# Kernel tuning notes

Measured on AMD Instinct MI355X. Metric: run time of the kernel, lower is better.

## Reference

```python
import jax, jax.numpy as jnp
import numpy as np

B, T, DM, H, HD = 2, 2048, 1024, 16, 64

def _rope_cos_sin(t, hd):
    inv_freq = 1.0 / (10000.0 ** (jnp.arange(0, hd, 2, dtype=jnp.float32) / hd))
    ang = jnp.arange(t, dtype=jnp.float32)[:, None] * inv_freq[None, :]  # [T, hd/2]
    emb = jnp.concatenate([ang, ang], axis=-1)  # [T, hd]
    return jnp.cos(emb), jnp.sin(emb)

def setup_inputs() -> dict:
    key = jax.random.key(0)
    kx, kq, kp = jax.random.split(key, 3)
    x = jax.random.normal(kx, (B, T, DM), dtype=jnp.float32)
    cos, sin = _rope_cos_sin(T, HD)
    w_qkv = jax.random.normal(kq, (3 * DM, DM), dtype=jnp.float32) * (DM ** -0.5)
    w_proj = jax.random.normal(kp, (DM, DM), dtype=jnp.float32) * (DM ** -0.5)
    return {"x": x, "cos": cos, "sin": sin, "w_qkv": w_qkv, "w_proj": w_proj}

def _rotate_half(u):
    d = u.shape[-1] // 2
    return jnp.concatenate([-u[..., d:], u[..., :d]], axis=-1)

def _apply_rope(u, cos, sin):
    # u: [B, T, H, D]; cos/sin: [T, D] -> unsqueeze_dim=1 -> [T, 1, D]
    c = cos[:, None, :]
    s = sin[:, None, :]
    return u * c + _rotate_half(u) * s

def reference(x, cos, sin, w_qkv, w_proj):
    b, t, _ = x.shape
    qkv = jnp.einsum('btd,ed->bte', x, w_qkv)            # [B, T, 3*DM]
    qkv = qkv.reshape(b, t, 3, H, HD)
    q, k, v = qkv[:, :, 0], qkv[:, :, 1], qkv[:, :, 2]   # each [B, T, H, HD]
    q = _apply_rope(q, cos, sin)
    k = _apply_rope(k, cos, sin)
    q = q.transpose(0, 2, 1, 3)                          # [B, H, T, HD]
    k = k.transpose(0, 2, 1, 3)
    v = v.transpose(0, 2, 1, 3)
    scale = 1.0 / jnp.sqrt(jnp.float32(HD))
    scores = jnp.einsum('bhqd,bhkd->bhqk', q, k) * scale  # [B, H, T, T]
    causal = jnp.tril(jnp.ones((t, t), dtype=bool))
    scores = jnp.where(causal[None, None], scores, jnp.finfo(scores.dtype).min)
    attn = jax.nn.softmax(scores, axis=-1)
    out = jnp.einsum('bhqk,bhkd->bhqd', attn, v)          # [B, H, T, HD]
    out = out.transpose(0, 2, 1, 3).reshape(b, t, H * HD)
    return jnp.einsum('btd,ed->bte', out, w_proj)
```

## Files before the change

### kernel.cpp

```cpp
#include <hip/hip_runtime.h>
#include <stdint.h>

#define Bb 2
#define Tt 2048
#define DMm 1024
#define Hh 16
#define HDd 64
#define Mrows (Bb*Tt)

typedef __attribute__((ext_vector_type(8)))  __bf16 bf16x8;
typedef __attribute__((ext_vector_type(4)))  __bf16 bf16x4;
typedef __attribute__((ext_vector_type(4)))  float  f32x4;
typedef __attribute__((ext_vector_type(16))) float  f32x16;
typedef __attribute__((ext_vector_type(4)))  unsigned int u32x4;
typedef __attribute__((ext_vector_type(2)))  unsigned int u32x2;

#define GLD16(gp, lp) __builtin_amdgcn_global_load_lds( \
    (const __attribute__((address_space(1))) unsigned int*)(gp), \
    (__attribute__((address_space(3))) unsigned int*)(lp), 16, 0, 0)

static __device__ __forceinline__ unsigned cvtpk_bf16(float lo, float hi) {
  unsigned r;
  asm("v_cvt_pk_bf16_f32 %0, %1, %2" : "=v"(r) : "v"(lo), "v"(hi));
  return r;
}
static __device__ __forceinline__ float exp2_hw(float x) {
  float r;
  asm("v_exp_f32 %0, %1" : "=v"(r) : "v"(x));
  return r;
}
static __device__ __forceinline__ float fmax3(float a, float b, float c) {
  return fmaxf(fmaxf(a, b), c);
}
static __device__ __forceinline__ float xmax32(float v) {
  return fmaxf(v, __shfl_xor(v, 32));
}
static __device__ __forceinline__ float xsum32(float v) {
  return v + __shfl_xor(v, 32);
}

__global__ __launch_bounds__(256)
void cast3_k(const float* __restrict__ a, const float* __restrict__ b,
             const float* __restrict__ c,
             __bf16* __restrict__ oa, __bf16* __restrict__ ob,
             __bf16* __restrict__ oc,
             const float* __restrict__ cosb, const float* __restrict__ sinb,
             unsigned* __restrict__ cs) {
  const int NA = 1048576, NB = 786432, NC = 262144;
  int i = blockIdx.x * 256 + threadIdx.x;
  if (i < NA + NB + NC) {
    const float* src; __bf16* dst; int k;
    if (i < NA)            { src = a; dst = oa; k = i; }
    else if (i < NA + NB)  { src = b; dst = ob; k = i - NA; }
    else                   { src = c; dst = oc; k = i - NA - NB; }
    float4 v = ((const float4*)src)[k];
    bf16x4 o;
    o[0] = (__bf16)v.x; o[1] = (__bf16)v.y; o[2] = (__bf16)v.z; o[3] = (__bf16)v.w;
    ((bf16x4*)dst)[k] = o;
  } else {
    int k = i - (NA + NB + NC);
    cs[k] = cvtpk_bf16(cosb[k], sinb[k]);
  }
}

__global__ __launch_bounds__(256)
void gemm_bt(const __bf16* __restrict__ A, const __bf16* __restrict__ Bm,
             float* __restrict__ C) {
  const int N = 1024, K = 1024;
  __shared__ __bf16 As[128 * 32];
  __shared__ __bf16 Bs[64 * 32];
  const int bid = blockIdx.x;
  const int xcd = bid & 7, i2 = bid >> 3;
  const int rowBase = (xcd * 4 + (i2 & 3)) * 128;
  const int colBase = (i2 >> 2) * 64;
  const int tid  = threadIdx.x;
  const int lane = tid & 63, wid = tid >> 6;
  const int l4 = lane & 15, lhi = lane >> 4;
  const int wh = wid >> 1, ww = wid & 1;
  f32x4 acc[4][2] = {};
  const int e0 = wid * 512 + lane * 8;
  const int r0 = e0 >> 5, c0 = e0 & 31;
  const __bf16* a0 = A  + (size_t)(rowBase + r0)      * K + c0;
  const __bf16* a1 = A  + (size_t)(rowBase + r0 + 64) * K + c0;
  const __bf16* b0 = Bm + (size_t)(colBase + r0)      * K + c0;
  for (int k0 = 0; k0 < K; k0 += 32) {
    __syncthreads();
    GLD16(a0 + k0, &As[wid * 512]);
    GLD16(a1 + k0, &As[2048 + wid * 512]);
    GLD16(b0 + k0, &Bs[wid * 512]);
    __syncthreads();
    bf16x8 af[4], bfr[2];
#pragma unroll
    for (int i = 0; i < 4; i++)
      af[i]  = *(const bf16x8*)&As[(wh * 64 + i * 16 + l4) * 32 + lhi * 8];
#pragma unroll
    for (int j = 0; j < 2; j++)
      bfr[j] = *(const bf16x8*)&Bs[(ww * 32 + j * 16 + l4) * 32 + lhi * 8];
#pragma unroll
    for (int i = 0; i < 4; i++)
#pragma unroll
      for (int j = 0; j < 2; j++)
        acc[i][j] = __builtin_amdgcn_mfma_f32_16x16x32_bf16(af[i], bfr[j], acc[i][j], 0, 0, 0);
  }
#pragma unroll
  for (int i = 0; i < 4; i++) {
    int R = rowBase + wh * 64 + i * 16 + lhi * 4;
#pragma unroll
    for (int j = 0; j < 2; j++) {
      int Cc = colBase + ww * 32 + j * 16 + l4;
      float* cp = C + (size_t)R * N + Cc;
#pragma unroll
      for (int q = 0; q < 4; q++) cp[(size_t)q * N] = acc[i][j][q];
    }
  }
}

__global__ __launch_bounds__(256)
void gemm_qkv(const __bf16* __restrict__ A, const __bf16* __restrict__ Bm,
              __bf16* __restrict__ Qb, __bf16* __restrict__ Kb,
              __bf16* __restrict__ Vfb, const unsigned* __restrict__ csb) {
  const int K = 1024;
  __shared__ __bf16 ldsu[16384];
  __bf16* As = ldsu;
  __bf16* Bs = ldsu + 4096;
  const int bid = blockIdx.x;
  const int xcd = bid & 7, i2 = bid >> 3;
  const int rowBase = (xcd * 4 + (i2 & 3)) * 128;
  const int colBase = (i2 >> 2) * 128;
  const int tid  = threadIdx.x;
  const int lane = tid & 63, wid = tid >> 6;
  const int l4 = lane & 15, lhi = lane >> 4;
  const int wh = wid >> 1, ww = wid & 1;
  f32x4 acc[4][4] = {};
  const int e0 = wid * 512 + lane * 8;
  const int r0 = e0 >> 5, c0 = e0 & 31;
  const __bf16* a0 = A  + (size_t)(rowBase + r0)      * K + c0;
  const __bf16* a1 = A  + (size_t)(rowBase + r0 + 64) * K + c0;
  const __bf16* b0 = Bm + (size_t)(colBase + r0)      * K + c0;
  const __bf16* b1 = Bm + (size_t)(colBase + r0 + 64) * K + c0;
  for (int k0 = 0; k0 < K; k0 += 32) {
    __syncthreads();
    GLD16(a0 + k0, &As[wid * 512]);
    GLD16(a1 + k0, &As[2048 + wid * 512]);
    GLD16(b0 + k0, &Bs[wid * 512]);
    GLD16(b1 + k0, &Bs[2048 + wid * 512]);
    __syncthreads();
    bf16x8 af[4], bfr[4];
#pragma unroll
    for (int i = 0; i < 4; i++) {
      af[i]  = *(const bf16x8*)&As[(wh * 64 + i * 16 + l4) * 32 + lhi * 8];
      bfr[i] = *(const bf16x8*)&Bs[(ww * 64 + i * 16 + l4) * 32 + lhi * 8];
    }
#pragma unroll
    for (int i = 0; i < 4; i++)
#pragma unroll
      for (int j = 0; j < 4; j++)
        acc[i][j] = __builtin_amdgcn_mfma_f32_16x16x32_bf16(af[i], bfr[j], acc[i][j], 0, 0, 0);
  }

  const int region = colBase >> 10;
  const int base_h = (colBase & 1023) >> 6;
  const int bIdx   = rowBase >> 11;
  const int tileBase = (rowBase & 2047) >> 5;

  __syncthreads();

  if (region < 2) {
    const float qscale = region ? 1.f : 0.18033688f;
#pragma unroll
    for (int i = 0; i < 4; i++) {
      const int tbase = ww * 8192 + (wh * 2 + (i >> 1)) * 2048;
      const int rsub  = (i & 1) * 16 + lhi * 4;
      const int trow0 = (rowBase & 2047) + wh * 64 + i * 16 + lhi * 4;
#pragma unroll
      for (int j = 0; j < 4; j++) {
        int dd = j * 16 + l4;
        float sg = (j < 2) ? -1.f : 1.f;
        int lbase = tbase + j * 512 + (l4 >> 3) * 256 + (l4 & 7);
#pragma unroll
        for (int q = 0; q < 4; q++) {
          unsigned cw = csb[(trow0 + q) * 64 + dd];
          float cc = __builtin_bit_cast(float, cw << 16);
          float sn = __builtin_bit_cast(float, cw & 0xffff0000u);
          float r = (acc[i][j][q] * cc + sg * acc[i][j ^ 2][q] * sn) * qscale;
          ldsu[lbase + (rsub + q) * 8] = (__bf16)r;
        }
      }
    }
  } else {
#pragma unroll
    for (int i = 0; i < 4; i++) {
      const int tbase = ww * 8192 + (wh * 2 + (i >> 1)) * 2048 + (i & 1) * 512;
#pragma unroll
      for (int j = 0; j < 4; j++) {
        int lbase = tbase + (j >> 1) * 1024 + ((j & 1) * 16 + l4) * 8;
#pragma unroll
        for (int q = 0; q < 4; q++) {
          int rq = lhi * 4 + q;
          ldsu[lbase + ((rq >> 3) & 1) * 256 + (rq & 7)] = (__bf16)acc[i][j][q];
        }
      }
    }
  }
  __syncthreads();

  __bf16* dstBuf = (region == 0) ? Qb : (region == 1 ? Kb : Vfb);
#pragma unroll
  for (int h2 = 0; h2 < 2; ++h2) {
    __bf16* dst = dstBuf + (size_t)(bIdx * 16 + base_h + h2) * (Tt * 64)
                + (size_t)tileBase * 2048;
#pragma unroll
    for (int k = 0; k < 4; ++k) {
      int eoff = k * 2048 + tid * 8;
      *(bf16x8*)(dst + eoff) = *(const bf16x8*)&ldsu[h2 * 8192 + eoff];
    }
  }
}

__global__ __launch_bounds__(256)
void attn_k(const __bf16* __restrict__ Q, const __bf16* __restrict__ K,
            const __bf16* __restrict__ Vb, __bf16* __restrict__ O) {
  const int bid = blockIdx.x;
  const int xcd = bid & 7;
  const int ii  = bid >> 3;
  const int bh  = xcd * 4 + (ii & 3);
  const int jj  = ii >> 2;
  const int b = bh >> 4, h = bh & 15;
  const int tid = threadIdx.x, lane = tid & 63, w = tid >> 6;
  const int l5 = lane & 31, hi = lane >> 5;
  const size_t baseF = (size_t)bh * (Tt * 64);
  const int laneoff = (hi << 8) + (l5 << 3);
  const float NEG_INF = -__builtin_inff();

  __shared__ float  oL[4][32][65];
  __shared__ float2 msL[4][32];

#define FRAGP(P, tile, c) ((P) + baseF + (size_t)(((tile) * 4 + (c)) << 9) + laneoff)

#define LOADK(KA, TIX) do {                                               \
    KA[0] = *(const bf16x8*)FRAGP(K, (TIX), 0);                           \
    KA[1] = *(const bf16x8*)FRAGP(K, (TIX), 1);                           \
    KA[2] = *(const bf16x8*)FRAGP(K, (TIX), 2);                           \
    KA[3] = *(const bf16x8*)FRAGP(K, (TIX), 3);                           \
  } while (0)
#define LOADV(TIX) do {                                                   \
    vc[0] = *(const bf16x8*)FRAGP(Vb, (TIX), 0);                          \
    vc[1] = *(const bf16x8*)FRAGP(Vb, (TIX), 1);                          \
    vc[2] = *(const bf16x8*)FRAGP(Vb, (TIX), 2);                          \
    vc[3] = *(const bf16x8*)FRAGP(Vb, (TIX), 3);                          \
  } while (0)

#define COMPUTE(KA, TIX) do {                                             \
    f32x16 s = {};                                                        \
    __builtin_amdgcn_s_setprio(1);                                        \
    s = __builtin_amdgcn_mfma_f32_32x32x16_bf16(KA[0], qf[0], s, 0, 0, 0);\
    s = __builtin_amdgcn_mfma_f32_32x32x16_bf16(KA[1], qf[1], s, 0, 0, 0);\
    s = __builtin_amdgcn_mfma_f32_32x32x16_bf16(KA[2], qf[2], s, 0, 0, 0);\
    s = __builtin_amdgcn_mfma_f32_32x32x16_bf16(KA[3], qf[3], s, 0, 0, 0);\
    __builtin_amdgcn_s_setprio(0);                                        \
    if ((TIX) == qsub) {                                                  \
      _Pragma("unroll")                                                   \
      for (int r = 0; r < 16; r++) {                                      \
        int kof = (r & 3) + 8 * (r >> 2) + 4 * hi;                        \
        s[r] = (kof <= l5) ? s[r] : NEG_INF;                              \
      }                                                                   \
    }                                                                     \
    float t0 = fmax3(s[0], s[1], s[2]);                                   \
    float t1 = fmax3(s[3], s[4], s[5]);                                   \
    float t2 = fmax3(s[6], s[7], s[8]);                                   \
    float t3 = fmax3(s[9], s[10], s[11]);                                 \
    float t4 = fmax3(s[12], s[13], s[14]);                                \
    float pmax = fmaxf(fmax3(t0, t1, t2), fmax3(t3, t4, s[15]));          \
    pmax = xmax32(pmax);                                                  \
    if (__any(pmax > m + 11.5f)) {                                        \
      float mn = fmaxf(m, pmax);                                          \
      float al = exp2_hw(m - mn);                                         \
      m = mn;                                                             \
      ssum *= al;                                                         \
      float arow[16];                                                     \
      _Pragma("unroll")                                                   \
      for (int r = 0; r < 16; r++)                                        \
        arow[r] = __shfl(al, (r & 3) + 8 * (r >> 2) + 4 * hi);            \
      _Pragma("unroll")                                                   \
      for (int r = 0; r < 16; r++) { o0[r] *= arow[r]; o1[r] *= arow[r]; }\
    }                                                                     \
    float p[16], rsl = 0.f;                                               \
    _Pragma("unroll")                                                     \
    for (int r = 0; r < 16; r++) { p[r] = exp2_hw(s[r] - m); rsl += p[r]; } \
    ssum += xsum32(rsl);                                                  \
    bf16x8 pa[2];                                                         \
    _Pragma("unroll")                                                     \
    for (int kc = 0; kc < 2; kc++) {                                      \
      const float* pp = p + kc * 8;                                       \
      unsigned X0 = cvtpk_bf16(pp[0], pp[1]);                             \
      unsigned Y0 = cvtpk_bf16(pp[4], pp[5]);                             \
      unsigned X1 = cvtpk_bf16(pp[2], pp[3]);                             \
      unsigned Y1 = cvtpk_bf16(pp[6], pp[7]);                             \
      u32x2 q0 = __builtin_amdgcn_permlane32_swap(X0, Y0, false, false);  \
      u32x2 q1 = __builtin_amdgcn_permlane32_swap(X1, Y1, false, false);  \
      u32x4 pw;                                                           \
      pw[0] = q0[0]; pw[1] = q1[0]; pw[2] = q0[1]; pw[3] = q1[1];         \
      pa[kc] = __builtin_bit_cast(bf16x8, pw);                            \
    }                                                                     \
    __builtin_amdgcn_s_setprio(1);                                        \
    o0 = __builtin_amdgcn_mfma_f32_32x32x16_bf16(pa[0], vc[0], o0, 0, 0, 0);\
    o0 = __builtin_amdgcn_mfma_f32_32x32x16_bf16(pa[1], vc[1], o0, 0, 0, 0);\
    o1 = __builtin_amdgcn_mfma_f32_32x32x16_bf16(pa[0], vc[2], o1, 0, 0, 0);\
    o1 = __builtin_amdgcn_mfma_f32_32x32x16_bf16(pa[1], vc[3], o1, 0, 0, 0);\
    __builtin_amdgcn_s_setprio(0);                                        \
  } while (0)

#define TCLAMP(tx) ( ((tx) > qsub) ? qsub : (tx) )

  for (int ph = 0; ph < 2; ++ph) {
    const int qsub  = ph ? (63 - jj) : jj;
    const int qrow0 = qsub * 32;

    bf16x8 qf[4];
#pragma unroll
    for (int cc = 0; cc < 4; cc++)
      qf[cc] = *(const bf16x8*)FRAGP(Q, qsub, cc);

    f32x16 o0 = {}, o1 = {};
    float m = NEG_INF, ssum = 0.f;

    const int NT = qsub + 1;
    const int dtw = NT - w;
    const int n = (dtw > 0) ? ((dtw + 3) >> 2) : 0;

    bf16x8 kA[4], kB[4], vc[4];

    LOADK(kA, TCLAMP(w));
    int i = 0;
    for (; i + 2 <= n; i += 2) {
      LOADV(w + 4 * i);
      LOADK(kB, TCLAMP(w + 4 * i + 4));
      COMPUTE(kA, w + 4 * i);
      LOADV(w + 4 * i + 4);
      LOADK(kA, TCLAMP(w + 4 * i + 8));
      COMPUTE(kB, w + 4 * i + 4);
    }
    if (i < n) {
      LOADV(w + 4 * i);
      COMPUTE(kA, w + 4 * i);
    }

#pragma unroll
    for (int r = 0; r < 16; r++) {
      int row = (r & 3) + 8 * (r >> 2) + 4 * hi;
      oL[w][row][l5]      = o0[r];
      oL[w][row][32 + l5] = o1[r];
    }
    if (hi == 0) msL[w][l5] = make_float2(m, ssum);
    __syncthreads();

    {
      const int row = l5;
      const int dbase = w * 16 + hi * 8;
      float2 s0 = msL[0][row], s1 = msL[1][row], s2 = msL[2][row], s3 = msL[3][row];
      float M = fmaxf(fmaxf(s0.x, s1.x), fmaxf(s2.x, s3.x));
      float a0 = exp2_hw(s0.x - M), a1 = exp2_hw(s1.x - M);
      float a2 = exp2_hw(s2.x - M), a3 = exp2_hw(s3.x - M);
      float inv = 1.f / (a0 * s0.y + a1 * s1.y + a2 * s2.y + a3 * s3.y);
      bf16x8 ov;
#pragma unroll
      for (int e = 0; e < 8; e++) {
        float v = a0 * oL[0][row][dbase + e] + a1 * oL[1][row][dbase + e]
                + a2 * oL[2][row][dbase + e] + a3 * oL[3][row][dbase + e];
        ov[e] = (__bf16)(v * inv);
      }
      *(bf16x8*)(O + ((size_t)b * Tt + qrow0 + row) * DMm + h * 64 + dbase) = ov;
    }
    __syncthreads();
  }
}

extern "C" void kernel_launch(void* const* d_in, const int* in_sizes, int n_in,
                              void* d_out, int out_size, void* d_ws, size_t ws_size,
                              hipStream_t stream) {
  const float* x     = (const float*)d_in[0];
  const float* cosb  = (const float*)d_in[1];
  const float* sinb  = (const float*)d_in[2];
  const float* wqkv  = (const float*)d_in[3];
  const float* wproj = (const float*)d_in[4];
  float* out = (float*)d_out;

  char* ws = (char*)d_ws;
  __bf16*   xb     = (__bf16*)(ws + 0);
  __bf16*   wqkvb  = (__bf16*)(ws + 8388608);
  __bf16*   wprojb = (__bf16*)(ws + 14680064);
  unsigned* csb    = (unsigned*)(ws + 16777216);
  __bf16*   Qb     = (__bf16*)(ws + 17825792);
  __bf16*   Kb     = (__bf16*)(ws + 26214400);
  __bf16*   Vfb    = (__bf16*)(ws + 34603008);
  __bf16*   attno  = (__bf16*)(ws + 42991616);

  cast3_k<<<8704, 256, 0, stream>>>(x, wqkv, wproj, xb, wqkvb, wprojb,
                                    cosb, sinb, csb);

  gemm_qkv<<<768, 256, 0, stream>>>(xb, wqkvb, Qb, Kb, Vfb, csb);

  attn_k<<<1024, 256, 0, stream>>>(Qb, Kb, Vfb, attno);

  gemm_bt<<<512, 256, 0, stream>>>(attno, wprojb, out);
}
```

Baseline: 99.19 us.

## Software-pipeline QK^T MFMA one tile ahead of softmax and PV

```diff
diff --git a/kernel.cpp b/kernel.cpp
--- a/kernel.cpp
+++ b/kernel.cpp
@@ -250,27 +250,30 @@
     vc[3] = *(const bf16x8*)FRAGP(Vb, (TIX), 3);                          \
   } while (0)
 
-#define COMPUTE(KA, TIX) do {                                             \
-    f32x16 s = {};                                                        \
+#define QKT(SREG, KA) do {                                                \
+    SREG = (f32x16){};                                                    \
     __builtin_amdgcn_s_setprio(1);                                        \
-    s = __builtin_amdgcn_mfma_f32_32x32x16_bf16(KA[0], qf[0], s, 0, 0, 0);\
-    s = __builtin_amdgcn_mfma_f32_32x32x16_bf16(KA[1], qf[1], s, 0, 0, 0);\
-    s = __builtin_amdgcn_mfma_f32_32x32x16_bf16(KA[2], qf[2], s, 0, 0, 0);\
-    s = __builtin_amdgcn_mfma_f32_32x32x16_bf16(KA[3], qf[3], s, 0, 0, 0);\
+    SREG = __builtin_amdgcn_mfma_f32_32x32x16_bf16(KA[0], qf[0], SREG, 0, 0, 0);\
+    SREG = __builtin_amdgcn_mfma_f32_32x32x16_bf16(KA[1], qf[1], SREG, 0, 0, 0);\
+    SREG = __builtin_amdgcn_mfma_f32_32x32x16_bf16(KA[2], qf[2], SREG, 0, 0, 0);\
+    SREG = __builtin_amdgcn_mfma_f32_32x32x16_bf16(KA[3], qf[3], SREG, 0, 0, 0);\
     __builtin_amdgcn_s_setprio(0);                                        \
+  } while (0)
+
+#define FINISH(SREG, TIX) do {                                            \
     if ((TIX) == qsub) {                                                  \
       _Pragma("unroll")                                                   \
       for (int r = 0; r < 16; r++) {                                      \
         int kof = (r & 3) + 8 * (r >> 2) + 4 * hi;                        \
-        s[r] = (kof <= l5) ? s[r] : NEG_INF;                              \
+        SREG[r] = (kof <= l5) ? SREG[r] : NEG_INF;                        \
       }                                                                   \
     }                                                                     \
-    float t0 = fmax3(s[0], s[1], s[2]);                                   \
-    float t1 = fmax3(s[3], s[4], s[5]);                                   \
-    float t2 = fmax3(s[6], s[7], s[8]);                                   \
-    float t3 = fmax3(s[9], s[10], s[11]);                                 \
-    float t4 = fmax3(s[12], s[13], s[14]);                                \
-    float pmax = fmaxf(fmax3(t0, t1, t2), fmax3(t3, t4, s[15]));          \
+    float t0 = fmax3(SREG[0], SREG[1], SREG[2]);                          \
+    float t1 = fmax3(SREG[3], SREG[4], SREG[5]);                          \
+    float t2 = fmax3(SREG[6], SREG[7], SREG[8]);                          \
+    float t3 = fmax3(SREG[9], SREG[10], SREG[11]);                        \
+    float t4 = fmax3(SREG[12], SREG[13], SREG[14]);                       \
+    float pmax = fmaxf(fmax3(t0, t1, t2), fmax3(t3, t4, SREG[15]));       \
     pmax = xmax32(pmax);                                                  \
     if (__any(pmax > m + 11.5f)) {                                        \
       float mn = fmaxf(m, pmax);                                          \
@@ -286,7 +289,7 @@
     }                                                                     \
     float p[16], rsl = 0.f;                                               \
     _Pragma("unroll")                                                     \
-    for (int r = 0; r < 16; r++) { p[r] = exp2_hw(s[r] - m); rsl += p[r]; } \
+    for (int r = 0; r < 16; r++) { p[r] = exp2_hw(SREG[r] - m); rsl += p[r]; } \
     ssum += xsum32(rsl);                                                  \
     bf16x8 pa[2];                                                         \
     _Pragma("unroll")                                                     \
@@ -329,20 +332,26 @@
     const int n = (dtw > 0) ? ((dtw + 3) >> 2) : 0;
 
     bf16x8 kA[4], kB[4], vc[4];
-
-    LOADK(kA, TCLAMP(w));
-    int i = 0;
-    for (; i + 2 <= n; i += 2) {
-      LOADV(w + 4 * i);
-      LOADK(kB, TCLAMP(w + 4 * i + 4));
-      COMPUTE(kA, w + 4 * i);
-      LOADV(w + 4 * i + 4);
-      LOADK(kA, TCLAMP(w + 4 * i + 8));
-      COMPUTE(kB, w + 4 * i + 4);
-    }
-    if (i < n) {
-      LOADV(w + 4 * i);
-      COMPUTE(kA, w + 4 * i);
+    f32x16 sA, sB;
+
+    if (n > 0) {
+      LOADK(kA, TCLAMP(w));
+      QKT(sA, kA);
+      int i = 0;
+      for (; i + 2 <= n; i += 2) {
+        LOADV(w + 4 * i);
+        LOADK(kB, TCLAMP(w + 4 * i + 4));
+        QKT(sB, kB);
+        FINISH(sA, w + 4 * i);
+        LOADV(w + 4 * i + 4);
+        LOADK(kA, TCLAMP(w + 4 * i + 8));
+        QKT(sA, kA);
+        FINISH(sB, w + 4 * i + 4);
+      }
+      if (i < n) {
+        LOADV(w + 4 * i);
+        FINISH(sA, w + 4 * i);
+      }
     }
 
 #pragma unroll
```

After: 101.6 us. +2.4%, slower.
